# Kernel tuning notes

Hardware: AMD Instinct MI355X
Metric: run time of the kernel (lower is better)

## Reference

```python
import jax, jax.numpy as jnp
import numpy as np

_EPS = 1e-5

def _block(x, g, b, W, bias):
    # BatchNorm1d (training-mode batch stats, biased variance) -> Linear -> ReLU; Dropout treated as identity (eval)
    m = jnp.mean(x, axis=0)
    v = jnp.mean((x - m) ** 2, axis=0)
    xn = (x - m) * jax.lax.rsqrt(v + _EPS) * g + b
    return jax.nn.relu(xn @ W + bias)

def _seg_mean(h, dst, n):
    # DGL mean reducer: 0 for nodes with no in-edges
    s = jax.ops.segment_sum(h, dst, num_segments=n)
    c = jax.ops.segment_sum(jnp.ones((h.shape[0], 1), h.dtype), dst, num_segments=n)
    return s / jnp.maximum(c, 1.0)

def setup_inputs() -> dict:
    key = jax.random.key(0)
    ks = iter(jax.random.split(key, 64))
    N, E, F, D = 20000, 300000, 128, 128
    d = {}
    d['win_f'] = jax.random.normal(next(ks), (E, F), jnp.float32)
    d['loss_f'] = jax.random.normal(next(ks), (E, F), jnp.float32)
    for name, din, dout in [('wi', F, D), ('li', F, D), ('src', D, D), ('dst', D, D), ('wl', D, D), ('ll', D, D), ('out', 2 * D, D)]:
        d[name + '_g'] = jnp.ones((din,), jnp.float32)
        d[name + '_b'] = jnp.zeros((din,), jnp.float32)
        d[name + '_W'] = jax.random.normal(next(ks), (din, dout), jnp.float32) * 0.05
        d[name + '_bias'] = jnp.zeros((dout,), jnp.float32)
    for name in ['win_src', 'win_dst', 'loss_src', 'loss_dst']:
        d[name] = jax.random.randint(next(ks), (E,), 0, N, jnp.int32)
    d['n_nodes'] = N
    return d

def reference(win_f, loss_f,
              wi_g, wi_b, wi_W, wi_bias,
              li_g, li_b, li_W, li_bias,
              src_g, src_b, src_W, src_bias,
              dst_g, dst_b, dst_W, dst_bias,
              wl_g, wl_b, wl_W, wl_bias,
              ll_g, ll_b, ll_W, ll_bias,
              out_g, out_b, out_W, out_bias,
              win_src, win_dst, loss_src, loss_dst, n_nodes):
    DEPTH = 3
    hw = _block(win_f, wi_g, wi_b, wi_W, wi_bias)   # [Ew, D]
    hl = _block(loss_f, li_g, li_b, li_W, li_bias)  # [El, D]
    # edge_to_node: per-etype scatter-mean, cross-type mean over the 2 etypes
    h = 0.5 * (_seg_mean(hw, win_dst, n_nodes) + _seg_mean(hl, loss_dst, n_nodes))  # [N, D]
    f = h
    for _ in range(DEPTH):
        hu = _block(h, src_g, src_b, src_W, src_bias)
        hv = _block(h, dst_g, dst_b, dst_W, dst_bias)
        hw = hu[win_src] + hv[win_dst]
        hl = hu[loss_src] + hv[loss_dst] # u_add_v on 'loss' edges
        hw = _block(hw, wl_g, wl_b, wl_W, wl_bias)
        hl = _block(hl, ll_g, ll_b, ll_W, ll_bias)
        h = 0.5 * (_seg_mean(hw, win_dst, n_nodes) + _seg_mean(hl, loss_dst, n_nodes))
    return _block(jnp.concatenate([f, h], axis=1), out_g, out_b, out_W, out_bias)
```

## Files before the change

### kernel.cpp

```cpp
#include <hip/hip_runtime.h>

#define NPART_MAX 2048

typedef __attribute__((ext_vector_type(8))) short short8;
typedef __attribute__((ext_vector_type(4))) float f32x4;

__device__ __forceinline__ float bf2f(uint u) {
    union { uint u; float f; } v; v.u = u << 16; return v.f;
}
__device__ __forceinline__ ushort f2bf(float f) {
    union { float f; uint u; } v; v.f = f;
    uint r = v.u + 0x7fffu + ((v.u >> 16) & 1u);
    return (ushort)(r >> 16);
}

__global__ __launch_bounds__(256) void hist2(const int* __restrict__ dw, const int* __restrict__ dl,
                                             int E, int* __restrict__ cw, int* __restrict__ cl) {
    const int half = gridDim.x >> 1;
    const bool second = (int)blockIdx.x >= half;
    const int* dst = second ? dl : dw;
    int* cnt = second ? cl : cw;
    const int b = second ? blockIdx.x - half : blockIdx.x;
    for (int e = b * 256 + threadIdx.x; e < E; e += half * 256)
        atomicAdd(&cnt[dst[e]], 1);
}

__global__ __launch_bounds__(256) void scan2(const int* __restrict__ cw, const int* __restrict__ cl,
                                             int n, int* offw, int* curw, int* offl, int* curl) {
    const int* cnt = blockIdx.x ? cl : cw;
    int* off = blockIdx.x ? offl : offw;
    int* cur = blockIdx.x ? curl : curw;
    __shared__ int warpsums[4];
    __shared__ int s_carry;
    if (threadIdx.x == 0) s_carry = 0;
    __syncthreads();
    for (int base = 0; base < n; base += 1024) {
        int i0 = base + threadIdx.x * 4;
        int v0 = (i0 + 0 < n) ? cnt[i0 + 0] : 0;
        int v1 = (i0 + 1 < n) ? cnt[i0 + 1] : 0;
        int v2 = (i0 + 2 < n) ? cnt[i0 + 2] : 0;
        int v3 = (i0 + 3 < n) ? cnt[i0 + 3] : 0;
        int tsum = v0 + v1 + v2 + v3;
        int lane = threadIdx.x & 63, w = threadIdx.x >> 6;
        int x = tsum;
        for (int d = 1; d < 64; d <<= 1) {
            int y = __shfl_up(x, d);
            if (lane >= d) x += y;
        }
        if (lane == 63) warpsums[w] = x;
        __syncthreads();
        int woff = 0;
        for (int k = 0; k < w; ++k) woff += warpsums[k];
        int excl = x - tsum + woff + s_carry;
        if (i0 + 0 < n) { off[i0 + 0] = excl; cur[i0 + 0] = excl; } excl += v0;
        if (i0 + 1 < n) { off[i0 + 1] = excl; cur[i0 + 1] = excl; } excl += v1;
        if (i0 + 2 < n) { off[i0 + 2] = excl; cur[i0 + 2] = excl; } excl += v2;
        if (i0 + 3 < n) { off[i0 + 3] = excl; cur[i0 + 3] = excl; } excl += v3;
        __syncthreads();
        if (threadIdx.x == 255) s_carry = excl;
        __syncthreads();
    }
    if (threadIdx.x == 0) off[n] = s_carry;
}

__global__ __launch_bounds__(256) void scatter2(
    const int* __restrict__ sw, const int* __restrict__ dw,
    const int* __restrict__ sl, const int* __restrict__ dl, int E,
    int* __restrict__ curw, int* __restrict__ curl,
    int* __restrict__ ipermw, int* __restrict__ ssrcw, int* __restrict__ sdstw,
    int* __restrict__ iperml, int* __restrict__ ssrcl, int* __restrict__ sdstl) {
    const int half = gridDim.x >> 1;
    const bool second = (int)blockIdx.x >= half;
    const int* src = second ? sl : sw;
    const int* dst = second ? dl : dw;
    int* cursor = second ? curl : curw;
    int* iperm = second ? iperml : ipermw;
    int* ssrc = second ? ssrcl : ssrcw;
    int* sdst = second ? sdstl : sdstw;
    const int b = second ? blockIdx.x - half : blockIdx.x;
    for (int e = b * 256 + threadIdx.x; e < E; e += half * 256) {
        int d = dst[e];
        int p = atomicAdd(&cursor[d], 1);
        iperm[e] = p;
        ssrc[p] = src[e];
        sdst[p] = d;
    }
}

__device__ __forceinline__ void convert_body(
    int b, int nb, const float4* __restrict__ x4, const int* __restrict__ iperm, int M,
    uint2* __restrict__ xb4, float* __restrict__ psum, float* __restrict__ psq) {
    const int cg = threadIdx.x & 31;
    const int sub = threadIdx.x >> 5;
    float s0=0,s1=0,s2=0,s3=0,q0=0,q1=0,q2=0,q3=0;
    for (int r = b * 8 + sub; r < M; r += nb * 8) {
        float4 v = x4[(size_t)r * 32 + cg];
        int p = iperm[r];
        uint2 o;
        o.x = (uint)f2bf(v.x) | ((uint)f2bf(v.y) << 16);
        o.y = (uint)f2bf(v.z) | ((uint)f2bf(v.w) << 16);
        xb4[(size_t)p * 32 + cg] = o;
        s0 += v.x; q0 += v.x * v.x;
        s1 += v.y; q1 += v.y * v.y;
        s2 += v.z; q2 += v.z * v.z;
        s3 += v.w; q3 += v.w * v.w;
    }
    __shared__ float rs[256][4], rq[256][4];
    rs[threadIdx.x][0]=s0; rs[threadIdx.x][1]=s1; rs[threadIdx.x][2]=s2; rs[threadIdx.x][3]=s3;
    rq[threadIdx.x][0]=q0; rq[threadIdx.x][1]=q1; rq[threadIdx.x][2]=q2; rq[threadIdx.x][3]=q3;
    __syncthreads();
    if (sub == 0) {
        #pragma unroll
        for (int k = 1; k < 8; ++k) {
            s0 += rs[k*32+cg][0]; s1 += rs[k*32+cg][1];
            s2 += rs[k*32+cg][2]; s3 += rs[k*32+cg][3];
            q0 += rq[k*32+cg][0]; q1 += rq[k*32+cg][1];
            q2 += rq[k*32+cg][2]; q3 += rq[k*32+cg][3];
        }
        psum[b*128 + cg*4+0] = s0; psq[b*128 + cg*4+0] = q0;
        psum[b*128 + cg*4+1] = s1; psq[b*128 + cg*4+1] = q1;
        psum[b*128 + cg*4+2] = s2; psq[b*128 + cg*4+2] = q2;
        psum[b*128 + cg*4+3] = s3; psq[b*128 + cg*4+3] = q3;
    }
}

__global__ __launch_bounds__(256) void convert_one(
    const float4* x4, const int* iperm, int M, uint2* xb4, float* psum, float* psq) {
    convert_body(blockIdx.x, gridDim.x, x4, iperm, M, xb4, psum, psq);
}

__global__ __launch_bounds__(256) void convert_two(
    const float4* x4a, const int* iperma, uint2* xb4a, float* psuma, float* psqa,
    const float4* x4b, const int* ipermb, uint2* xb4b, float* psumb, float* psqb, int M) {
    const int half = gridDim.x >> 1;
    const bool second = (int)blockIdx.x >= half;
    const int b = second ? blockIdx.x - half : blockIdx.x;
    convert_body(b, half,
                 second ? x4b : x4a, second ? ipermb : iperma, M,
                 second ? xb4b : xb4a, second ? psumb : psuma, second ? psqb : psqa);
}

__global__ __launch_bounds__(256) void colstats_b128(const uint* __restrict__ x2, int M,
                                                     float* __restrict__ psum, float* __restrict__ psq) {
    const int cl = threadIdx.x & 63;
    const int sub = threadIdx.x >> 6;
    float s0=0,s1=0,q0=0,q1=0;
    for (int r = blockIdx.x * 4 + sub; r < M; r += gridDim.x * 4) {
        uint u = x2[(size_t)r * 64 + cl];
        float a = bf2f(u & 0xffffu), b = bf2f(u >> 16);
        s0 += a; q0 += a * a;
        s1 += b; q1 += b * b;
    }
    __shared__ float red[4][64][4];
    red[sub][cl][0]=s0; red[sub][cl][1]=s1; red[sub][cl][2]=q0; red[sub][cl][3]=q1;
    __syncthreads();
    if (sub == 0) {
        #pragma unroll
        for (int k = 1; k < 4; ++k) {
            s0 += red[k][cl][0]; s1 += red[k][cl][1];
            q0 += red[k][cl][2]; q1 += red[k][cl][3];
        }
        psum[blockIdx.x*128 + 2*cl]   = s0; psq[blockIdx.x*128 + 2*cl]   = q0;
        psum[blockIdx.x*128 + 2*cl+1] = s1; psq[blockIdx.x*128 + 2*cl+1] = q1;
    }
}

__global__ __launch_bounds__(256) void colstats_b256(const uint* __restrict__ x2, int M,
                                                     float* __restrict__ psum, float* __restrict__ psq) {
    const int cl = threadIdx.x & 127;
    const int sub = threadIdx.x >> 7;
    float s0=0,s1=0,q0=0,q1=0;
    for (int r = blockIdx.x * 2 + sub; r < M; r += gridDim.x * 2) {
        uint u = x2[(size_t)r * 128 + cl];
        float a = bf2f(u & 0xffffu), b = bf2f(u >> 16);
        s0 += a; q0 += a * a;
        s1 += b; q1 += b * b;
    }
    __shared__ float red[2][128][4];
    red[sub][cl][0]=s0; red[sub][cl][1]=s1; red[sub][cl][2]=q0; red[sub][cl][3]=q1;
    __syncthreads();
    if (sub == 0) {
        s0 += red[1][cl][0]; s1 += red[1][cl][1];
        q0 += red[1][cl][2]; q1 += red[1][cl][3];
        psum[blockIdx.x*256 + 2*cl]   = s0; psq[blockIdx.x*256 + 2*cl]   = q0;
        psum[blockIdx.x*256 + 2*cl+1] = s1; psq[blockIdx.x*256 + 2*cl+1] = q1;
    }
}

__global__ __launch_bounds__(256) void gather_stats2(
    const uint2* __restrict__ hu4, const uint2* __restrict__ hv4,
    const int* __restrict__ sw, const int* __restrict__ dw,
    float* __restrict__ psumW, float* __restrict__ psqW,
    const int* __restrict__ sl, const int* __restrict__ dl,
    float* __restrict__ psumL, float* __restrict__ psqL, int E) {
    const int gh = gridDim.x >> 1;
    const bool second = (int)blockIdx.x >= gh;
    const int* sidx = second ? sl : sw;
    const int* didx = second ? dl : dw;
    float* psum = second ? psumL : psumW;
    float* psq  = second ? psqL  : psqW;
    const int b = second ? blockIdx.x - gh : blockIdx.x;

    const int lane = threadIdx.x & 63;
    const int w = threadIdx.x >> 6;
    const int half = lane >> 5;
    const int cg = lane & 31;
    const int gwave = (b * 256 + threadIdx.x) >> 6;
    const int nwave = (gh * 256) >> 6;
    float s0=0,s1=0,s2=0,s3=0,q0=0,q1=0,q2=0,q3=0;
    for (int base = gwave * 64; base < E; base += nwave * 64) {
        int e = base + lane;
        int su = (e < E) ? sidx[e] : 0;
        int dv = (e < E) ? didx[e] : 0;
        int cnt = min(64, E - base);
        int curd = -1;
        float hv0=0,hv1=0,hv2=0,hv3=0;
        float rs0=0,rs1=0,rs2=0,rs3=0,rq0=0,rq1=0,rq2=0,rq3=0,rlen=0;
        auto flush = [&]() {
            if (curd >= 0) {
                s0 += rs0 + rlen*hv0; q0 += rq0 + 2.f*hv0*rs0 + rlen*hv0*hv0;
                s1 += rs1 + rlen*hv1; q1 += rq1 + 2.f*hv1*rs1 + rlen*hv1*hv1;
                s2 += rs2 + rlen*hv2; q2 += rq2 + 2.f*hv2*rs2 + rlen*hv2*hv2;
                s3 += rs3 + rlen*hv3; q3 += rq3 + 2.f*hv3*rs3 + rlen*hv3*hv3;
            }
        };
        #pragma unroll 4
        for (int j = 0; j < 32; ++j) {
            int eidx = 2 * j + half;
            int a = __shfl(su, eidx), dd = __shfl(dv, eidx);
            if (eidx < cnt) {
                if (dd != curd) {
                    flush();
                    curd = dd;
                    uint2 vv = hv4[(size_t)dd * 32 + cg];
                    hv0 = bf2f(vv.x & 0xffffu); hv1 = bf2f(vv.x >> 16);
                    hv2 = bf2f(vv.y & 0xffffu); hv3 = bf2f(vv.y >> 16);
                    rs0=rs1=rs2=rs3=0; rq0=rq1=rq2=rq3=0; rlen=0;
                }
                uint2 uu = hu4[(size_t)a * 32 + cg];
                float u0 = bf2f(uu.x & 0xffffu), u1 = bf2f(uu.x >> 16);
                float u2 = bf2f(uu.y & 0xffffu), u3 = bf2f(uu.y >> 16);
                rs0 += u0; rq0 += u0*u0;
                rs1 += u1; rq1 += u1*u1;
                rs2 += u2; rq2 += u2*u2;
                rs3 += u3; rq3 += u3*u3;
                rlen += 1.f;
            }
        }
        flush();
    }
    __shared__ float redS[8][32][4], redQ[8][32][4];
    const int ri = w * 2 + half;
    redS[ri][cg][0]=s0; redS[ri][cg][1]=s1; redS[ri][cg][2]=s2; redS[ri][cg][3]=s3;
    redQ[ri][cg][0]=q0; redQ[ri][cg][1]=q1; redQ[ri][cg][2]=q2; redQ[ri][cg][3]=q3;
    __syncthreads();
    if (threadIdx.x < 128) {
        int c = threadIdx.x;
        int cgg = c >> 2, k = c & 3;
        float s = 0.f, q = 0.f;
        #pragma unroll
        for (int i = 0; i < 8; ++i) { s += redS[i][cgg][k]; q += redQ[i][cgg][k]; }
        psum[(size_t)b * 128 + c] = s;
        psq [(size_t)b * 128 + c] = q;
    }
}

__device__ __forceinline__ void reduce_body(
    int c, const float* __restrict__ psum, const float* __restrict__ psq,
    int nblk, int C, int M,
    const float* __restrict__ g1, const float* __restrict__ b1,
    float* __restrict__ scale1, float* __restrict__ shift1,
    const float* g2, const float* b2, float* scale2, float* shift2) {
    double s = 0.0, q = 0.0;
    for (int i = threadIdx.x; i < nblk; i += 256) {
        s += (double)psum[(size_t)i * C + c];
        q += (double)psq [(size_t)i * C + c];
    }
    __shared__ double ss[256], qs[256];
    ss[threadIdx.x] = s; qs[threadIdx.x] = q;
    __syncthreads();
    for (int d = 128; d > 0; d >>= 1) {
        if (threadIdx.x < d) {
            ss[threadIdx.x] += ss[threadIdx.x + d];
            qs[threadIdx.x] += qs[threadIdx.x + d];
        }
        __syncthreads();
    }
    if (threadIdx.x == 0) {
        double m = ss[0] / (double)M;
        double v = qs[0] / (double)M - m * m;
        if (v < 0.0) v = 0.0;
        double rs = 1.0 / sqrt(v + 1e-5);
        float mf = (float)m;
        float sc1 = (float)(rs * (double)g1[c]);
        scale1[c] = sc1;
        shift1[c] = b1[c] - mf * sc1;
        if (g2) {
            float sc2 = (float)(rs * (double)g2[c]);
            scale2[c] = sc2;
            shift2[c] = b2[c] - mf * sc2;
        }
    }
}

__global__ __launch_bounds__(256) void reduce_stats(
    const float* psum, const float* psq, int nblk, int C, int M,
    const float* g1, const float* b1, float* scale1, float* shift1,
    const float* g2, const float* b2, float* scale2, float* shift2) {
    reduce_body(blockIdx.x, psum, psq, nblk, C, M, g1, b1, scale1, shift1, g2, b2, scale2, shift2);
}

__global__ __launch_bounds__(256) void reduce_stats2(
    const float* psumA, const float* psqA, int nblkA, int CA, int MA,
    const float* gA, const float* bA, float* scaleA, float* shiftA,
    const float* psumB, const float* psqB, int nblkB, int CB, int MB,
    const float* gB, const float* bB, float* scaleB, float* shiftB) {
    if ((int)blockIdx.x < CA)
        reduce_body(blockIdx.x, psumA, psqA, nblkA, CA, MA, gA, bA, scaleA, shiftA,
                    nullptr, nullptr, nullptr, nullptr);
    else
        reduce_body(blockIdx.x - CA, psumB, psqB, nblkB, CB, MB, gB, bB, scaleB, shiftB,
                    nullptr, nullptr, nullptr, nullptr);
}

__device__ __forceinline__ void fold_body(
    int b, const float* __restrict__ scale, const float* __restrict__ shift, int C,
    const float* __restrict__ W, const float* __restrict__ bias,
    ushort* __restrict__ Wp, float* __restrict__ beff) {
    const int KT = C / 32;
    __shared__ float slab[32 * 128];
    if (b < KT) {
        const int kt = b;
        for (int i = threadIdx.x; i < 32 * 128; i += 256) {
            int kr = i >> 7, d = i & 127;
            int c = kt * 32 + kr;
            slab[i] = W[(size_t)c * 128 + d] * scale[c];
        }
        __syncthreads();
        #pragma unroll
        for (int t0 = 0; t0 < 512; t0 += 256) {
            int t = t0 + threadIdx.x;
            int lane = t & 63, dt = t >> 6;
            int d = dt * 16 + (lane & 15);
            int kb = (lane >> 4) * 8;
            uint4 o;
            o.x = (uint)f2bf(slab[(kb+0)*128 + d]) | ((uint)f2bf(slab[(kb+1)*128 + d]) << 16);
            o.y = (uint)f2bf(slab[(kb+2)*128 + d]) | ((uint)f2bf(slab[(kb+3)*128 + d]) << 16);
            o.z = (uint)f2bf(slab[(kb+4)*128 + d]) | ((uint)f2bf(slab[(kb+5)*128 + d]) << 16);
            o.w = (uint)f2bf(slab[(kb+6)*128 + d]) | ((uint)f2bf(slab[(kb+7)*128 + d]) << 16);
            *(uint4*)(Wp + (size_t)((dt * KT + kt) * 64 + lane) * 8) = o;
        }
    } else {
        const int bb = b - KT;
        const int dl = threadIdx.x & 15, ci = threadIdx.x >> 4;
        const int d = bb * 16 + dl;
        float a = 0.f;
        for (int c = ci; c < C; c += 16)
            a += shift[c] * W[(size_t)c * 128 + d];
        float* red = slab;
        red[threadIdx.x] = a;
        __syncthreads();
        if (ci == 0) {
            #pragma unroll
            for (int k = 1; k < 16; ++k) a += red[k * 16 + dl];
            beff[d] = bias[d] + a;
        }
    }
}

__global__ __launch_bounds__(256) void pack_fold_par(
    const float* scale, const float* shift, int C,
    const float* W, const float* bias, ushort* Wp, float* beff) {
    fold_body(blockIdx.x, scale, shift, C, W, bias, Wp, beff);
}

__global__ __launch_bounds__(256) void pack_fold2(
    const float* scaleA, const float* shiftA, int CA, const float* WA, const float* biasA,
    ushort* WpA, float* beffA,
    const float* scaleB, const float* shiftB, int CB, const float* WB, const float* biasB,
    ushort* WpB, float* beffB) {
    const int nA = CA / 32 + 8;
    const bool second = (int)blockIdx.x >= nA;
    fold_body(second ? blockIdx.x - nA : blockIdx.x,
              second ? scaleB : scaleA, second ? shiftB : shiftA, second ? CB : CA,
              second ? WB : WA, second ? biasB : biasA,
              second ? WpB : WpA, second ? beffB : beffA);
}

template<int KT, int MODE>
__device__ __forceinline__ void gemm_body(
    int b, const ushort* __restrict__ X,
    const ushort* __restrict__ Wp, const float* __restrict__ beff,
    ushort* __restrict__ Yb, float* __restrict__ Yf, int M) {
    constexpr int K = KT * 32;
    const int lane = threadIdx.x & 63;
    const int w = threadIdx.x >> 6;
    const int r0 = b * 128 + w * 32;
    const int rlo = lane & 15, khi = lane >> 4;

    f32x4 acc[2][8];
    #pragma unroll
    for (int rt = 0; rt < 2; ++rt)
        #pragma unroll
        for (int dt = 0; dt < 8; ++dt)
            acc[rt][dt] = (f32x4){0.f, 0.f, 0.f, 0.f};

    int row[2], idx[2];
    bool ok[2];
    #pragma unroll
    for (int rt = 0; rt < 2; ++rt) {
        row[rt] = r0 + rt * 16 + rlo;
        ok[rt] = row[rt] < M;
        idx[rt] = ok[rt] ? row[rt] : 0;
    }

    for (int kt = 0; kt < KT; ++kt) {
        short8 wf[8];
        #pragma unroll
        for (int dt = 0; dt < 8; ++dt)
            wf[dt] = *(const short8*)(Wp + (size_t)((dt * KT + kt) * 64 + lane) * 8);
        #pragma unroll
        for (int rt = 0; rt < 2; ++rt) {
            short8 bv = *(const short8*)(X + (size_t)idx[rt] * K + kt * 32 + khi * 8);
            #pragma unroll
            for (int dt = 0; dt < 8; ++dt)
                acc[rt][dt] = __builtin_amdgcn_mfma_f32_16x16x32_bf16(wf[dt], bv, acc[rt][dt], 0, 0, 0);
        }
    }

    #pragma unroll
    for (int rt = 0; rt < 2; ++rt) {
        if (!ok[rt]) continue;
        #pragma unroll
        for (int dt = 0; dt < 8; ++dt) {
            float v0, v1, v2, v3;
            if constexpr (MODE == 2) {
                v0 = acc[rt][dt][0]; v1 = acc[rt][dt][1];
                v2 = acc[rt][dt][2]; v3 = acc[rt][dt][3];
            } else {
                const float4 bz = *(const float4*)(beff + dt * 16 + khi * 4);
                v0 = fmaxf(acc[rt][dt][0] + bz.x, 0.f);
                v1 = fmaxf(acc[rt][dt][1] + bz.y, 0.f);
                v2 = fmaxf(acc[rt][dt][2] + bz.z, 0.f);
                v3 = fmaxf(acc[rt][dt][3] + bz.w, 0.f);
            }
            if constexpr (MODE == 1) {
                *(float4*)(Yf + (size_t)row[rt] * 128 + dt * 16 + khi * 4) = make_float4(v0, v1, v2, v3);
            } else {
                uint2 pk;
                pk.x = (uint)f2bf(v0) | ((uint)f2bf(v1) << 16);
                pk.y = (uint)f2bf(v2) | ((uint)f2bf(v3) << 16);
                *(uint2*)(Yb + (size_t)row[rt] * 128 + dt * 16 + khi * 4) = pk;
            }
        }
    }
}

__global__ __launch_bounds__(256) void gemm_final(
    const ushort* X, const ushort* Wp, const float* beff, float* Yf, int M) {
    gemm_body<8, 1>(blockIdx.x, X, Wp, beff, nullptr, Yf, M);
}

__global__ __launch_bounds__(256) void gemm_dual(
    const ushort* X,
    const ushort* Wp1, const float* beff1, ushort* Y1,
    const ushort* Wp2, const float* beff2, ushort* Y2, int M) {
    const int half = gridDim.x >> 1;
    const bool second = (int)blockIdx.x >= half;
    gemm_body<4, 0>(second ? blockIdx.x - half : blockIdx.x, X,
                    second ? Wp2 : Wp1, second ? beff2 : beff1,
                    second ? Y2 : Y1, nullptr, M);
}

__global__ __launch_bounds__(256) void gemm_quad(
    const ushort* hu, const ushort* hv,
    const ushort* Wp1, const ushort* Wp2,
    ushort* HUw, ushort* HVw, ushort* HUl, ushort* HVl, int M) {
    const int gq = gridDim.x >> 2;
    const int q = blockIdx.x / gq;
    const int b = blockIdx.x - q * gq;
    const ushort* X = (q & 1) ? hv : hu;
    const ushort* Wp = (q >= 2) ? Wp2 : Wp1;
    ushort* Y = (q == 0) ? HUw : (q == 1) ? HVw : (q == 2) ? HUl : HVl;
    gemm_body<4, 2>(b, X, Wp, nullptr, Y, nullptr, M);
}

__device__ __forceinline__ void gemm_seg_body(
    int b, const ushort* __restrict__ X,
    const int* __restrict__ sdst, const int* __restrict__ cnt,
    const ushort* __restrict__ Wp, const float* __restrict__ beff,
    float* __restrict__ hacc, int M) {
    constexpr int KT = 4;
    __shared__ ushort tile[64 * 132];
    __shared__ int   s_node[64];
    __shared__ float s_scale[64];
    const int tid = threadIdx.x;
    const int lane = tid & 63;
    const int w = tid >> 6;
    const int rb = b * 64;
    const int rlo = lane & 15, khi = lane >> 4;

    if (tid < 64) {
        int r = rb + tid;
        int nd = (r < M) ? sdst[r] : -1;
        s_node[tid] = nd;
        s_scale[tid] = (nd >= 0) ? 0.5f / fmaxf((float)cnt[nd], 1.f) : 0.f;
    }

    f32x4 acc[8];
    #pragma unroll
    for (int dt = 0; dt < 8; ++dt)
        acc[dt] = (f32x4){0.f, 0.f, 0.f, 0.f};

    const int row = rb + w * 16 + rlo;
    const bool ok = row < M;
    const int idx = ok ? row : 0;

    for (int kt = 0; kt < KT; ++kt) {
        short8 bv = *(const short8*)(X + (size_t)idx * 128 + kt * 32 + khi * 8);
        #pragma unroll 4
        for (int dt = 0; dt < 8; ++dt) {
            short8 wf = *(const short8*)(Wp + (size_t)((dt * KT + kt) * 64 + lane) * 8);
            acc[dt] = __builtin_amdgcn_mfma_f32_16x16x32_bf16(wf, bv, acc[dt], 0, 0, 0);
        }
    }

    const int rl = w * 16 + rlo;
    #pragma unroll
    for (int dt = 0; dt < 8; ++dt) {
        const float4 bz = *(const float4*)(beff + dt * 16 + khi * 4);
        float v0 = 0.f, v1 = 0.f, v2 = 0.f, v3 = 0.f;
        if (ok) {
            v0 = fmaxf(acc[dt][0] + bz.x, 0.f);
            v1 = fmaxf(acc[dt][1] + bz.y, 0.f);
            v2 = fmaxf(acc[dt][2] + bz.z, 0.f);
            v3 = fmaxf(acc[dt][3] + bz.w, 0.f);
        }
        uint2 pk;
        pk.x = (uint)f2bf(v0) | ((uint)f2bf(v1) << 16);
        pk.y = (uint)f2bf(v2) | ((uint)f2bf(v3) << 16);
        *(uint2*)&tile[rl * 132 + dt * 16 + khi * 4] = pk;
    }
    __syncthreads();

    const int col = tid & 127;
    const int rs = (tid >> 7) * 32;
    int cur = s_node[rs];
    float scl = s_scale[rs];
    float sum = 0.f;
    for (int r = rs; r < rs + 32; ++r) {
        int nd = s_node[r];
        if (nd != cur) {
            if (cur >= 0)
                atomicAdd(&hacc[(size_t)cur * 128 + col], sum * scl);
            cur = nd; scl = s_scale[r]; sum = 0.f;
        }
        sum += bf2f(tile[r * 132 + col]);
    }
    if (cur >= 0)
        atomicAdd(&hacc[(size_t)cur * 128 + col], sum * scl);
}

__global__ __launch_bounds__(256) void gemm_seg2(
    const ushort* XA, const int* sdstA, const int* cntA,
    const ushort* WpA, const float* beffA, int MA,
    const ushort* XB, const int* sdstB, const int* cntB,
    const ushort* WpB, const float* beffB, int MB,
    float* hacc) {
    const int half = gridDim.x >> 1;
    const bool second = (int)blockIdx.x >= half;
    gemm_seg_body(second ? blockIdx.x - half : blockIdx.x,
                  second ? XB : XA,
                  second ? sdstB : sdstA, second ? cntB : cntA,
                  second ? WpB : WpA, second ? beffB : beffA,
                  hacc, second ? MB : MA);
}

__global__ __launch_bounds__(256) void edge_seg2(
    const uint* __restrict__ HUw, const uint* __restrict__ HVw,
    const int* __restrict__ sw, const int* __restrict__ dw,
    const int* __restrict__ cw, const float* __restrict__ bw,
    const uint* __restrict__ HUl, const uint* __restrict__ HVl,
    const int* __restrict__ sl, const int* __restrict__ dl,
    const int* __restrict__ cl, const float* __restrict__ bl,
    float* __restrict__ hacc, int E) {
    const int gh = gridDim.x >> 1;
    const bool second = (int)blockIdx.x >= gh;
    const uint* HU = second ? HUl : HUw;
    const uint* HV = second ? HVl : HVw;
    const int* sidx = second ? sl : sw;
    const int* didx = second ? dl : dw;
    const int* cnt = second ? cl : cw;
    const float* beff = second ? bl : bw;
    const int b = second ? blockIdx.x - gh : blockIdx.x;

    const int lane = threadIdx.x & 63;
    const int gwave = (b * 256 + threadIdx.x) >> 6;
    const int nwave = (gh * 256) >> 6;
    const float bz0 = beff[2 * lane];
    const float bz1 = beff[2 * lane + 1];

    for (int base = gwave * 64; base < E; base += nwave * 64) {
        int e = base + lane;
        int su = (e < E) ? sidx[e] : 0;
        int dv = (e < E) ? didx[e] : 0;
        int cn = min(64, E - base);
        int cur = -1; float scl = 0.f, a0 = 0.f, a1 = 0.f, hv0 = 0.f, hv1 = 0.f;
        auto body = [&](int j) {
            int aa = __shfl(su, j), dd = __shfl(dv, j);
            if (dd != cur) {
                if (cur >= 0) {
                    atomicAdd(&hacc[(size_t)cur * 128 + 2 * lane],     a0 * scl);
                    atomicAdd(&hacc[(size_t)cur * 128 + 2 * lane + 1], a1 * scl);
                }
                cur = dd; scl = 0.5f / fmaxf((float)cnt[dd], 1.f); a0 = 0.f; a1 = 0.f;
                uint vv = HV[(size_t)dd * 64 + lane];
                hv0 = bf2f(vv & 0xffffu); hv1 = bf2f(vv >> 16);
            }
            uint uu = HU[(size_t)aa * 64 + lane];
            a0 += fmaxf(bf2f(uu & 0xffffu) + hv0 + bz0, 0.f);
            a1 += fmaxf(bf2f(uu >> 16)     + hv1 + bz1, 0.f);
        };
        if (cn == 64) {
            #pragma unroll 4
            for (int j = 0; j < 64; ++j) body(j);
        } else {
            for (int j = 0; j < cn; ++j) body(j);
        }
        if (cur >= 0) {
            atomicAdd(&hacc[(size_t)cur * 128 + 2 * lane],     a0 * scl);
            atomicAdd(&hacc[(size_t)cur * 128 + 2 * lane + 1], a1 * scl);
        }
    }
}

__global__ __launch_bounds__(256) void finalize_hacc(
    float2* __restrict__ hacc2, uint* __restrict__ h2, uint* __restrict__ fh2,
    int fhsel, int N) {
    const int total = N * 64;
    for (int i = blockIdx.x * 256 + threadIdx.x; i < total; i += gridDim.x * 256) {
        float2 v = hacc2[i];
        uint pk = (uint)f2bf(v.x) | ((uint)f2bf(v.y) << 16);
        h2[i] = pk;
        if (fhsel >= 0) fh2[((size_t)(i >> 6)) * 128 + fhsel * 64 + (i & 63)] = pk;
        hacc2[i] = make_float2(0.f, 0.f);
    }
}

extern "C" void kernel_launch(void* const* d_in, const int* in_sizes, int n_in,
                              void* d_out, int out_size, void* d_ws, size_t ws_size,
                              hipStream_t stream) {
    const float* win_f  = (const float*)d_in[0];
    const float* loss_f = (const float*)d_in[1];
    struct BP { const float *g, *b, *W, *bias; };
    auto bp = [&](int i) { return BP{ (const float*)d_in[i], (const float*)d_in[i+1],
                                      (const float*)d_in[i+2], (const float*)d_in[i+3] }; };
    BP wi = bp(2), li = bp(6), srcp = bp(10), dstp = bp(14), wl = bp(18), ll = bp(22), outp = bp(26);
    const int* win_src  = (const int*)d_in[30];
    const int* win_dst  = (const int*)d_in[31];
    const int* loss_src = (const int*)d_in[32];
    const int* loss_dst = (const int*)d_in[33];
    const int E = in_sizes[30];
    const int N = out_size / 128;
    (void)n_in;

    char* base = (char*)d_ws;
    size_t off_b = 0;
    auto alloc = [&](size_t bytes) {
        size_t cur = off_b;
        off_b += (bytes + 255) & ~(size_t)255;
        return (void*)(base + cur);
    };
    float*  hacc = (float*)alloc((size_t)N * 128 * 4);
    ushort* h    = (ushort*)alloc((size_t)N * 128 * 2);
    ushort* hu   = (ushort*)alloc((size_t)N * 128 * 2);
    ushort* hv   = (ushort*)alloc((size_t)N * 128 * 2);
    ushort* fh   = (ushort*)alloc((size_t)N * 256 * 2);
    ushort* HUw  = (ushort*)alloc((size_t)N * 128 * 2);
    ushort* HVw  = (ushort*)alloc((size_t)N * 128 * 2);
    ushort* HUl  = (ushort*)alloc((size_t)N * 128 * 2);
    ushort* HVl  = (ushort*)alloc((size_t)N * 128 * 2);
    int* cntw  = (int*)alloc((size_t)N * 4);
    int* cntl  = (int*)alloc((size_t)N * 4);
    int* offw  = (int*)alloc((size_t)(N + 1) * 4);
    int* offl  = (int*)alloc((size_t)(N + 1) * 4);
    int* curw  = (int*)alloc((size_t)N * 4);
    int* curl  = (int*)alloc((size_t)N * 4);
    int* ipermw= (int*)alloc((size_t)E * 4);
    int* ssrcw = (int*)alloc((size_t)E * 4);
    int* sdstw = (int*)alloc((size_t)E * 4);
    int* iperml= (int*)alloc((size_t)E * 4);
    int* ssrcl = (int*)alloc((size_t)E * 4);
    int* sdstl = (int*)alloc((size_t)E * 4);
    float* psumW = (float*)alloc((size_t)NPART_MAX * 128 * 4);
    float* psqW  = (float*)alloc((size_t)NPART_MAX * 128 * 4);
    float* psumL = (float*)alloc((size_t)NPART_MAX * 128 * 4);
    float* psqL  = (float*)alloc((size_t)NPART_MAX * 128 * 4);
    float* psumN = (float*)alloc((size_t)512 * 256 * 4);
    float* psqN  = (float*)alloc((size_t)512 * 256 * 4);
    float* scal1 = (float*)alloc(256 * 4);
    float* shif1 = (float*)alloc(256 * 4);
    float* scal2 = (float*)alloc(256 * 4);
    float* shif2 = (float*)alloc(256 * 4);
    ushort* Wp1 = (ushort*)alloc((size_t)256 * 128 * 2);
    ushort* Wp2 = (ushort*)alloc((size_t)256 * 128 * 2);
    float* beff1 = (float*)alloc(128 * 4);
    float* beff2 = (float*)alloc(128 * 4);
    ushort* Xbf1 = (ushort*)alloc((size_t)E * 128 * 2);
    if (off_b > ws_size) return;
    size_t off_one = off_b;
    ushort* Xbf2 = (ushort*)alloc((size_t)E * 128 * 2);
    const bool have_x2 = (off_b <= ws_size);
    if (!have_x2) off_b = off_one;

    const int gE64 = (E + 63) / 64;
    const int gN = (N + 127) / 128;
    const int NBF = 1024;
    const int NBG = 2048;
    const int NBN = 512;

    hipMemsetAsync(cntw, 0, (size_t)N * 4, stream);
    hipMemsetAsync(cntl, 0, (size_t)N * 4, stream);
    hipMemsetAsync(hacc, 0, (size_t)N * 128 * 4, stream);
    hist2<<<2048, 256, 0, stream>>>(win_dst, loss_dst, E, cntw, cntl);
    scan2<<<2, 256, 0, stream>>>(cntw, cntl, N, offw, curw, offl, curl);
    scatter2<<<2048, 256, 0, stream>>>(win_src, win_dst, loss_src, loss_dst, E,
                                       curw, curl, ipermw, ssrcw, sdstw, iperml, ssrcl, sdstl);

    if (have_x2) {
        convert_two<<<2 * NBF, 256, 0, stream>>>(
            (const float4*)win_f, ipermw, (uint2*)Xbf1, psumW, psqW,
            (const float4*)loss_f, iperml, (uint2*)Xbf2, psumL, psqL, E);
        reduce_stats2<<<256, 256, 0, stream>>>(
            psumW, psqW, NBF, 128, E, wi.g, wi.b, scal1, shif1,
            psumL, psqL, NBF, 128, E, li.g, li.b, scal2, shif2);
        pack_fold2<<<24, 256, 0, stream>>>(scal1, shif1, 128, wi.W, wi.bias, Wp1, beff1,
                                           scal2, shif2, 128, li.W, li.bias, Wp2, beff2);
        gemm_seg2<<<2 * gE64, 256, 0, stream>>>(
            Xbf1, sdstw, cntw, Wp1, beff1, E,
            Xbf2, sdstl, cntl, Wp2, beff2, E, hacc);
    } else {
        convert_one<<<NBF, 256, 0, stream>>>((const float4*)win_f, ipermw, E, (uint2*)Xbf1, psumW, psqW);
        reduce_stats<<<128, 256, 0, stream>>>(psumW, psqW, NBF, 128, E, wi.g, wi.b, scal1, shif1,
                                              nullptr, nullptr, nullptr, nullptr);
        pack_fold_par<<<12, 256, 0, stream>>>(scal1, shif1, 128, wi.W, wi.bias, Wp1, beff1);
        gemm_seg2<<<2 * gE64, 256, 0, stream>>>(
            Xbf1, sdstw, cntw, Wp1, beff1, E,
            Xbf1, sdstw, cntw, Wp1, beff1, 0, hacc);
        convert_one<<<NBF, 256, 0, stream>>>((const float4*)loss_f, iperml, E, (uint2*)Xbf1, psumW, psqW);
        reduce_stats<<<128, 256, 0, stream>>>(psumW, psqW, NBF, 128, E, li.g, li.b, scal1, shif1,
                                              nullptr, nullptr, nullptr, nullptr);
        pack_fold_par<<<12, 256, 0, stream>>>(scal1, shif1, 128, li.W, li.bias, Wp1, beff1);
        gemm_seg2<<<2 * gE64, 256, 0, stream>>>(
            Xbf1, sdstl, cntl, Wp1, beff1, E,
            Xbf1, sdstl, cntl, Wp1, beff1, 0, hacc);
    }
    finalize_hacc<<<512, 256, 0, stream>>>((float2*)hacc, (uint*)h, (uint*)fh, 0, N);

    for (int it = 0; it < 3; ++it) {
        colstats_b128<<<NBN, 256, 0, stream>>>((const uint*)h, N, psumN, psqN);
        reduce_stats<<<128, 256, 0, stream>>>(psumN, psqN, NBN, 128, N, srcp.g, srcp.b, scal1, shif1,
                                              dstp.g, dstp.b, scal2, shif2);
        pack_fold2<<<24, 256, 0, stream>>>(scal1, shif1, 128, srcp.W, srcp.bias, Wp1, beff1,
                                           scal2, shif2, 128, dstp.W, dstp.bias, Wp2, beff2);
        gemm_dual<<<2 * gN, 256, 0, stream>>>(h, Wp1, beff1, hu, Wp2, beff2, hv, N);

        gather_stats2<<<2 * NBG, 256, 0, stream>>>(
            (const uint2*)hu, (const uint2*)hv,
            ssrcw, sdstw, psumW, psqW, ssrcl, sdstl, psumL, psqL, E);
        reduce_stats2<<<256, 256, 0, stream>>>(
            psumW, psqW, NBG, 128, E, wl.g, wl.b, scal1, shif1,
            psumL, psqL, NBG, 128, E, ll.g, ll.b, scal2, shif2);
        pack_fold2<<<24, 256, 0, stream>>>(scal1, shif1, 128, wl.W, wl.bias, Wp1, beff1,
                                           scal2, shif2, 128, ll.W, ll.bias, Wp2, beff2);
        gemm_quad<<<4 * gN, 256, 0, stream>>>(hu, hv, Wp1, Wp2, HUw, HVw, HUl, HVl, N);
        edge_seg2<<<2 * NBG, 256, 0, stream>>>(
            (const uint*)HUw, (const uint*)HVw, ssrcw, sdstw, cntw, beff1,
            (const uint*)HUl, (const uint*)HVl, ssrcl, sdstl, cntl, beff2,
            hacc, E);
        finalize_hacc<<<512, 256, 0, stream>>>((float2*)hacc, (uint*)h, (uint*)fh,
                                               (it == 2) ? 1 : -1, N);
    }

    colstats_b256<<<NBN, 256, 0, stream>>>((const uint*)fh, N, psumN, psqN);
    reduce_stats<<<256, 256, 0, stream>>>(psumN, psqN, NBN, 256, N, outp.g, outp.b, scal1, shif1,
                                          nullptr, nullptr, nullptr, nullptr);
    pack_fold_par<<<16, 256, 0, stream>>>(scal1, shif1, 256, outp.W, outp.bias, Wp1, beff1);
    gemm_final<<<gN, 256, 0, stream>>>(fh, Wp1, beff1, (float*)d_out, N);
}
```

Measured before the change: 840.5 us.

## Gather fp32 edge features in GEMM via perm; fuse node stats into finalize

The separate conversion pass that wrote a permuted bf16 copy of the edge features is removed. The segment GEMM now gathers fp32 rows through a forward permutation and converts them to bf16 in registers, and a lighter stats-only kernel computes the column statistics. Column statistics for node features are computed inside the finalize kernel, which drops the standalone colstats passes. This saves a full write and re-read of the bf16 copy, in exchange for random fp32 row gathers in the GEMM, which read twice as many bytes per row. The stats now come from fp32 accumulators rather than the bf16-rounded values, which slightly changes numerics.

```diff
diff --git a/kernel.cpp b/kernel.cpp
--- a/kernel.cpp
+++ b/kernel.cpp
@@ -67,39 +67,34 @@
     const int* __restrict__ sw, const int* __restrict__ dw,
     const int* __restrict__ sl, const int* __restrict__ dl, int E,
     int* __restrict__ curw, int* __restrict__ curl,
-    int* __restrict__ ipermw, int* __restrict__ ssrcw, int* __restrict__ sdstw,
-    int* __restrict__ iperml, int* __restrict__ ssrcl, int* __restrict__ sdstl) {
+    int* __restrict__ permw, int* __restrict__ ssrcw, int* __restrict__ sdstw,
+    int* __restrict__ perml, int* __restrict__ ssrcl, int* __restrict__ sdstl) {
     const int half = gridDim.x >> 1;
     const bool second = (int)blockIdx.x >= half;
     const int* src = second ? sl : sw;
     const int* dst = second ? dl : dw;
     int* cursor = second ? curl : curw;
-    int* iperm = second ? iperml : ipermw;
+    int* perm = second ? perml : permw;
     int* ssrc = second ? ssrcl : ssrcw;
     int* sdst = second ? sdstl : sdstw;
     const int b = second ? blockIdx.x - half : blockIdx.x;
     for (int e = b * 256 + threadIdx.x; e < E; e += half * 256) {
         int d = dst[e];
         int p = atomicAdd(&cursor[d], 1);
-        iperm[e] = p;
+        perm[p] = e;
         ssrc[p] = src[e];
         sdst[p] = d;
     }
 }
 
-__device__ __forceinline__ void convert_body(
-    int b, int nb, const float4* __restrict__ x4, const int* __restrict__ iperm, int M,
-    uint2* __restrict__ xb4, float* __restrict__ psum, float* __restrict__ psq) {
+__device__ __forceinline__ void statsf_body(
+    int b, int nb, const float4* __restrict__ x4, int M,
+    float* __restrict__ psum, float* __restrict__ psq) {
     const int cg = threadIdx.x & 31;
     const int sub = threadIdx.x >> 5;
     float s0=0,s1=0,s2=0,s3=0,q0=0,q1=0,q2=0,q3=0;
     for (int r = b * 8 + sub; r < M; r += nb * 8) {
         float4 v = x4[(size_t)r * 32 + cg];
-        int p = iperm[r];
-        uint2 o;
-        o.x = (uint)f2bf(v.x) | ((uint)f2bf(v.y) << 16);
-        o.y = (uint)f2bf(v.z) | ((uint)f2bf(v.w) << 16);
-        xb4[(size_t)p * 32 + cg] = o;
         s0 += v.x; q0 += v.x * v.x;
         s1 += v.y; q1 += v.y * v.y;
         s2 += v.z; q2 += v.z * v.z;
@@ -124,67 +119,13 @@
     }
 }
 
-__global__ __launch_bounds__(256) void convert_one(
-    const float4* x4, const int* iperm, int M, uint2* xb4, float* psum, float* psq) {
-    convert_body(blockIdx.x, gridDim.x, x4, iperm, M, xb4, psum, psq);
-}
-
-__global__ __launch_bounds__(256) void convert_two(
-    const float4* x4a, const int* iperma, uint2* xb4a, float* psuma, float* psqa,
-    const float4* x4b, const int* ipermb, uint2* xb4b, float* psumb, float* psqb, int M) {
+__global__ __launch_bounds__(256) void stats_f32_2(
+    const float4* xa, float* psa, float* pqa,
+    const float4* xb, float* psb, float* pqb, int M) {
     const int half = gridDim.x >> 1;
     const bool second = (int)blockIdx.x >= half;
-    const int b = second ? blockIdx.x - half : blockIdx.x;
-    convert_body(b, half,
-                 second ? x4b : x4a, second ? ipermb : iperma, M,
-                 second ? xb4b : xb4a, second ? psumb : psuma, second ? psqb : psqa);
-}
-
-__global__ __launch_bounds__(256) void colstats_b128(const uint* __restrict__ x2, int M,
-                                                     float* __restrict__ psum, float* __restrict__ psq) {
-    const int cl = threadIdx.x & 63;
-    const int sub = threadIdx.x >> 6;
-    float s0=0,s1=0,q0=0,q1=0;
-    for (int r = blockIdx.x * 4 + sub; r < M; r += gridDim.x * 4) {
-        uint u = x2[(size_t)r * 64 + cl];
-        float a = bf2f(u & 0xffffu), b = bf2f(u >> 16);
-        s0 += a; q0 += a * a;
-        s1 += b; q1 += b * b;
-    }
-    __shared__ float red[4][64][4];
-    red[sub][cl][0]=s0; red[sub][cl][1]=s1; red[sub][cl][2]=q0; red[sub][cl][3]=q1;
-    __syncthreads();
-    if (sub == 0) {
-        #pragma unroll
-        for (int k = 1; k < 4; ++k) {
-            s0 += red[k][cl][0]; s1 += red[k][cl][1];
-            q0 += red[k][cl][2]; q1 += red[k][cl][3];
-        }
-        psum[blockIdx.x*128 + 2*cl]   = s0; psq[blockIdx.x*128 + 2*cl]   = q0;
-        psum[blockIdx.x*128 + 2*cl+1] = s1; psq[blockIdx.x*128 + 2*cl+1] = q1;
-    }
-}
-
-__global__ __launch_bounds__(256) void colstats_b256(const uint* __restrict__ x2, int M,
-                                                     float* __restrict__ psum, float* __restrict__ psq) {
-    const int cl = threadIdx.x & 127;
-    const int sub = threadIdx.x >> 7;
-    float s0=0,s1=0,q0=0,q1=0;
-    for (int r = blockIdx.x * 2 + sub; r < M; r += gridDim.x * 2) {
-        uint u = x2[(size_t)r * 128 + cl];
-        float a = bf2f(u & 0xffffu), b = bf2f(u >> 16);
-        s0 += a; q0 += a * a;
-        s1 += b; q1 += b * b;
-    }
-    __shared__ float red[2][128][4];
-    red[sub][cl][0]=s0; red[sub][cl][1]=s1; red[sub][cl][2]=q0; red[sub][cl][3]=q1;
-    __syncthreads();
-    if (sub == 0) {
-        s0 += red[1][cl][0]; s1 += red[1][cl][1];
-        q0 += red[1][cl][2]; q1 += red[1][cl][3];
-        psum[blockIdx.x*256 + 2*cl]   = s0; psq[blockIdx.x*256 + 2*cl]   = q0;
-        psum[blockIdx.x*256 + 2*cl+1] = s1; psq[blockIdx.x*256 + 2*cl+1] = q1;
-    }
+    statsf_body(second ? blockIdx.x - half : blockIdx.x, half,
+                second ? xb : xa, M, second ? psb : psa, second ? pqb : pqa);
 }
 
 __global__ __launch_bounds__(256) void gather_stats2(
@@ -486,7 +427,7 @@
 }
 
 __device__ __forceinline__ void gemm_seg_body(
-    int b, const ushort* __restrict__ X,
+    int b, const float* __restrict__ XF, const int* __restrict__ perm,
     const int* __restrict__ sdst, const int* __restrict__ cnt,
     const ushort* __restrict__ Wp, const float* __restrict__ beff,
     float* __restrict__ hacc, int M) {
@@ -514,10 +455,17 @@
 
     const int row = rb + w * 16 + rlo;
     const bool ok = row < M;
-    const int idx = ok ? row : 0;
+    const int pidx = ok ? perm[row] : 0;
 
     for (int kt = 0; kt < KT; ++kt) {
-        short8 bv = *(const short8*)(X + (size_t)idx * 128 + kt * 32 + khi * 8);
+        const float* p = XF + (size_t)pidx * 128 + kt * 32 + khi * 8;
+        float4 xa = *(const float4*)p;
+        float4 xb = *(const float4*)(p + 4);
+        short8 bv;
+        bv[0] = (short)f2bf(xa.x); bv[1] = (short)f2bf(xa.y);
+        bv[2] = (short)f2bf(xa.z); bv[3] = (short)f2bf(xa.w);
+        bv[4] = (short)f2bf(xb.x); bv[5] = (short)f2bf(xb.y);
+        bv[6] = (short)f2bf(xb.z); bv[7] = (short)f2bf(xb.w);
         #pragma unroll 4
         for (int dt = 0; dt < 8; ++dt) {
             short8 wf = *(const short8*)(Wp + (size_t)((dt * KT + kt) * 64 + lane) * 8);
@@ -562,15 +510,15 @@
 }
 
 __global__ __launch_bounds__(256) void gemm_seg2(
-    const ushort* XA, const int* sdstA, const int* cntA,
+    const float* XA, const int* permA, const int* sdstA, const int* cntA,
     const ushort* WpA, const float* beffA, int MA,
-    const ushort* XB, const int* sdstB, const int* cntB,
+    const float* XB, const int* permB, const int* sdstB, const int* cntB,
     const ushort* WpB, const float* beffB, int MB,
     float* hacc) {
     const int half = gridDim.x >> 1;
     const bool second = (int)blockIdx.x >= half;
     gemm_seg_body(second ? blockIdx.x - half : blockIdx.x,
-                  second ? XB : XA,
+                  second ? XB : XA, second ? permB : permA,
                   second ? sdstB : sdstA, second ? cntB : cntA,
                   second ? WpB : WpA, second ? beffB : beffA,
                   hacc, second ? MB : MA);
@@ -634,16 +582,43 @@
     }
 }
 
-__global__ __launch_bounds__(256) void finalize_hacc(
+__global__ __launch_bounds__(256) void finalize_hacc_stats(
     float2* __restrict__ hacc2, uint* __restrict__ h2, uint* __restrict__ fh2,
-    int fhsel, int N) {
-    const int total = N * 64;
-    for (int i = blockIdx.x * 256 + threadIdx.x; i < total; i += gridDim.x * 256) {
+    int fhsel, int N,
+    float* __restrict__ psA, float* __restrict__ pqA, int strideA, int offA,
+    float* __restrict__ psB, float* __restrict__ pqB, int strideB, int offB) {
+    const int cl = threadIdx.x & 63;
+    const int sub = threadIdx.x >> 6;
+    float s0=0,s1=0,q0=0,q1=0;
+    for (int n = blockIdx.x * 4 + sub; n < N; n += gridDim.x * 4) {
+        int i = n * 64 + cl;
         float2 v = hacc2[i];
         uint pk = (uint)f2bf(v.x) | ((uint)f2bf(v.y) << 16);
         h2[i] = pk;
-        if (fhsel >= 0) fh2[((size_t)(i >> 6)) * 128 + fhsel * 64 + (i & 63)] = pk;
+        if (fhsel >= 0) fh2[(size_t)n * 128 + fhsel * 64 + cl] = pk;
         hacc2[i] = make_float2(0.f, 0.f);
+        s0 += v.x; q0 += v.x * v.x;
+        s1 += v.y; q1 += v.y * v.y;
+    }
+    __shared__ float red[4][64][4];
+    red[sub][cl][0]=s0; red[sub][cl][1]=s1; red[sub][cl][2]=q0; red[sub][cl][3]=q1;
+    __syncthreads();
+    if (sub == 0) {
+        #pragma unroll
+        for (int k = 1; k < 4; ++k) {
+            s0 += red[k][cl][0]; s1 += red[k][cl][1];
+            q0 += red[k][cl][2]; q1 += red[k][cl][3];
+        }
+        psA[(size_t)blockIdx.x * strideA + offA + 2*cl]     = s0;
+        psA[(size_t)blockIdx.x * strideA + offA + 2*cl + 1] = s1;
+        pqA[(size_t)blockIdx.x * strideA + offA + 2*cl]     = q0;
+        pqA[(size_t)blockIdx.x * strideA + offA + 2*cl + 1] = q1;
+        if (psB) {
+            psB[(size_t)blockIdx.x * strideB + offB + 2*cl]     = s0;
+            psB[(size_t)blockIdx.x * strideB + offB + 2*cl + 1] = s1;
+            pqB[(size_t)blockIdx.x * strideB + offB + 2*cl]     = q0;
+            pqB[(size_t)blockIdx.x * strideB + offB + 2*cl + 1] = q1;
+        }
     }
 }
 
@@ -686,18 +661,20 @@
     int* offl  = (int*)alloc((size_t)(N + 1) * 4);
     int* curw  = (int*)alloc((size_t)N * 4);
     int* curl  = (int*)alloc((size_t)N * 4);
-    int* ipermw= (int*)alloc((size_t)E * 4);
+    int* permw = (int*)alloc((size_t)E * 4);
     int* ssrcw = (int*)alloc((size_t)E * 4);
     int* sdstw = (int*)alloc((size_t)E * 4);
-    int* iperml= (int*)alloc((size_t)E * 4);
+    int* perml = (int*)alloc((size_t)E * 4);
     int* ssrcl = (int*)alloc((size_t)E * 4);
     int* sdstl = (int*)alloc((size_t)E * 4);
     float* psumW = (float*)alloc((size_t)NPART_MAX * 128 * 4);
     float* psqW  = (float*)alloc((size_t)NPART_MAX * 128 * 4);
     float* psumL = (float*)alloc((size_t)NPART_MAX * 128 * 4);
     float* psqL  = (float*)alloc((size_t)NPART_MAX * 128 * 4);
-    float* psumN = (float*)alloc((size_t)512 * 256 * 4);
-    float* psqN  = (float*)alloc((size_t)512 * 256 * 4);
+    float* psumN = (float*)alloc((size_t)512 * 128 * 4);
+    float* psqN  = (float*)alloc((size_t)512 * 128 * 4);
+    float* psum256 = (float*)alloc((size_t)512 * 256 * 4);
+    float* psq256  = (float*)alloc((size_t)512 * 256 * 4);
     float* scal1 = (float*)alloc(256 * 4);
     float* shif1 = (float*)alloc(256 * 4);
     float* scal2 = (float*)alloc(256 * 4);
@@ -706,12 +683,7 @@
     ushort* Wp2 = (ushort*)alloc((size_t)256 * 128 * 2);
     float* beff1 = (float*)alloc(128 * 4);
     float* beff2 = (float*)alloc(128 * 4);
-    ushort* Xbf1 = (ushort*)alloc((size_t)E * 128 * 2);
     if (off_b > ws_size) return;
-    size_t off_one = off_b;
-    ushort* Xbf2 = (ushort*)alloc((size_t)E * 128 * 2);
-    const bool have_x2 = (off_b <= ws_size);
-    if (!have_x2) off_b = off_one;
 
     const int gE64 = (E + 63) / 64;
     const int gN = (N + 127) / 128;
@@ -725,40 +697,24 @@
     hist2<<<2048, 256, 0, stream>>>(win_dst, loss_dst, E, cntw, cntl);
     scan2<<<2, 256, 0, stream>>>(cntw, cntl, N, offw, curw, offl, curl);
     scatter2<<<2048, 256, 0, stream>>>(win_src, win_dst, loss_src, loss_dst, E,
-                                       curw, curl, ipermw, ssrcw, sdstw, iperml, ssrcl, sdstl);
-
-    if (have_x2) {
-        convert_two<<<2 * NBF, 256, 0, stream>>>(
-            (const float4*)win_f, ipermw, (uint2*)Xbf1, psumW, psqW,
-            (const float4*)loss_f, iperml, (uint2*)Xbf2, psumL, psqL, E);
-        reduce_stats2<<<256, 256, 0, stream>>>(
-            psumW, psqW, NBF, 128, E, wi.g, wi.b, scal1, shif1,
-            psumL, psqL, NBF, 128, E, li.g, li.b, scal2, shif2);
-        pack_fold2<<<24, 256, 0, stream>>>(scal1, shif1, 128, wi.W, wi.bias, Wp1, beff1,
-                                           scal2, shif2, 128, li.W, li.bias, Wp2, beff2);
-        gemm_seg2<<<2 * gE64, 256, 0, stream>>>(
-            Xbf1, sdstw, cntw, Wp1, beff1, E,
-            Xbf2, sdstl, cntl, Wp2, beff2, E, hacc);
-    } else {
-        convert_one<<<NBF, 256, 0, stream>>>((const float4*)win_f, ipermw, E, (uint2*)Xbf1, psumW, psqW);
-        reduce_stats<<<128, 256, 0, stream>>>(psumW, psqW, NBF, 128, E, wi.g, wi.b, scal1, shif1,
-                                              nullptr, nullptr, nullptr, nullptr);
-        pack_fold_par<<<12, 256, 0, stream>>>(scal1, shif1, 128, wi.W, wi.bias, Wp1, beff1);
-        gemm_seg2<<<2 * gE64, 256, 0, stream>>>(
-            Xbf1, sdstw, cntw, Wp1, beff1, E,
-            Xbf1, sdstw, cntw, Wp1, beff1, 0, hacc);
-        convert_one<<<NBF, 256, 0, stream>>>((const float4*)loss_f, iperml, E, (uint2*)Xbf1, psumW, psqW);
-        reduce_stats<<<128, 256, 0, stream>>>(psumW, psqW, NBF, 128, E, li.g, li.b, scal1, shif1,
-                                              nullptr, nullptr, nullptr, nullptr);
-        pack_fold_par<<<12, 256, 0, stream>>>(scal1, shif1, 128, li.W, li.bias, Wp1, beff1);
-        gemm_seg2<<<2 * gE64, 256, 0, stream>>>(
-            Xbf1, sdstl, cntl, Wp1, beff1, E,
-            Xbf1, sdstl, cntl, Wp1, beff1, 0, hacc);
-    }
-    finalize_hacc<<<512, 256, 0, stream>>>((float2*)hacc, (uint*)h, (uint*)fh, 0, N);
+                                       curw, curl, permw, ssrcw, sdstw, perml, ssrcl, sdstl);
+
+    stats_f32_2<<<2 * NBF, 256, 0, stream>>>(
+        (const float4*)win_f, psumW, psqW,
+        (const float4*)loss_f, psumL, psqL, E);
+    reduce_stats2<<<256, 256, 0, stream>>>(
+        psumW, psqW, NBF, 128, E, wi.g, wi.b, scal1, shif1,
+        psumL, psqL, NBF, 128, E, li.g, li.b, scal2, shif2);
+    pack_fold2<<<24, 256, 0, stream>>>(scal1, shif1, 128, wi.W, wi.bias, Wp1, beff1,
+                                       scal2, shif2, 128, li.W, li.bias, Wp2, beff2);
+    gemm_seg2<<<2 * gE64, 256, 0, stream>>>(
+        win_f, permw, sdstw, cntw, Wp1, beff1, E,
+        loss_f, perml, sdstl, cntl, Wp2, beff2, E, hacc);
+    finalize_hacc_stats<<<NBN, 256, 0, stream>>>(
+        (float2*)hacc, (uint*)h, (uint*)fh, 0, N,
+        psumN, psqN, 128, 0, psum256, psq256, 256, 0);
 
     for (int it = 0; it < 3; ++it) {
-        colstats_b128<<<NBN, 256, 0, stream>>>((const uint*)h, N, psumN, psqN);
         reduce_stats<<<128, 256, 0, stream>>>(psumN, psqN, NBN, 128, N, srcp.g, srcp.b, scal1, shif1,
                                               dstp.g, dstp.b, scal2, shif2);
         pack_fold2<<<24, 256, 0, stream>>>(scal1, shif1, 128, srcp.W, srcp.bias, Wp1, beff1,
@@ -778,12 +734,18 @@
             (const uint*)HUw, (const uint*)HVw, ssrcw, sdstw, cntw, beff1,
             (const uint*)HUl, (const uint*)HVl, ssrcl, sdstl, cntl, beff2,
             hacc, E);
-        finalize_hacc<<<512, 256, 0, stream>>>((float2*)hacc, (uint*)h, (uint*)fh,
-                                               (it == 2) ? 1 : -1, N);
-    }
-
-    colstats_b256<<<NBN, 256, 0, stream>>>((const uint*)fh, N, psumN, psqN);
-    reduce_stats<<<256, 256, 0, stream>>>(psumN, psqN, NBN, 256, N, outp.g, outp.b, scal1, shif1,
+        if (it < 2) {
+            finalize_hacc_stats<<<NBN, 256, 0, stream>>>(
+                (float2*)hacc, (uint*)h, (uint*)fh, -1, N,
+                psumN, psqN, 128, 0, nullptr, nullptr, 0, 0);
+        } else {
+            finalize_hacc_stats<<<NBN, 256, 0, stream>>>(
+                (float2*)hacc, (uint*)h, (uint*)fh, 1, N,
+                psum256, psq256, 256, 128, nullptr, nullptr, 0, 0);
+        }
+    }
+
+    reduce_stats<<<256, 256, 0, stream>>>(psum256, psq256, NBN, 256, N, outp.g, outp.b, scal1, shif1,
                                           nullptr, nullptr, nullptr, nullptr);
     pack_fold_par<<<16, 256, 0, stream>>>(scal1, shif1, 256, outp.W, outp.bias, Wp1, beff1);
     gemm_final<<<gN, 256, 0, stream>>>(fh, Wp1, beff1, (float*)d_out, N);
```

Result: faster. 810.3 us (-3.6%).
